# Optimization experiments

Hardware: AMD Instinct MI355X
Metric: run time of the kernel (lower is better)

## Reference

```python
import jax, jax.numpy as jnp
import numpy as np

N = 50000
E = 800000
IN_DIM = 256
HID = 64
HEADS = 4
OUT = 64
NEG_SLOPE = 0.2


def _gat_layer(x, src, dst, W, a_src, a_dst, b, heads, out_ch, concat):
    n = x.shape[0]
    h = (x @ W).reshape(n, heads, out_ch)                      # [N,H,C]
    al_src = jnp.sum(h * a_src, axis=-1)                       # [N,H]
    al_dst = jnp.sum(h * a_dst, axis=-1)                       # [N,H]
    e = jax.nn.leaky_relu(al_src[src] + al_dst[dst], NEG_SLOPE)  # [E,H]
    # segment softmax over destination nodes
    m = jax.ops.segment_max(e, dst, num_segments=n)
    m = jnp.where(jnp.isfinite(m), m, 0.0)
    ex = jnp.exp(e - m[dst])
    denom = jax.ops.segment_sum(ex, dst, num_segments=n)
    alpha = ex / (denom[dst] + 1e-16)                          # [E,H]
    msg = h[src] * alpha[:, :, None]                           # [E,H,C]
    out = jax.ops.segment_sum(msg, dst, num_segments=n)        # [N,H,C]
    out = out.reshape(n, heads * out_ch) if concat else out.mean(axis=1)
    return out + b


def setup_inputs() -> dict:
    key = jax.random.key(0)
    ks = jax.random.split(key, 16)
    x = jax.random.normal(ks[0], (N, IN_DIM), dtype=jnp.float32)
    edge_index = jax.random.randint(ks[1], (2, E), 0, N, dtype=jnp.int64)

    def glorot(k, shape):
        fan = shape[0] + shape[-1]
        s = jnp.sqrt(6.0 / fan).astype(jnp.float32)
        return jax.random.uniform(k, shape, jnp.float32, -s, s)

    # layer 1: IN_DIM -> HID x HEADS (concat)
    W1 = glorot(ks[2], (IN_DIM, HEADS * HID))
    a_src1 = glorot(ks[3], (HEADS, HID))
    a_dst1 = glorot(ks[4], (HEADS, HID))
    b1 = jnp.zeros((HEADS * HID,), jnp.float32)
    # layer 2: HID*HEADS -> HID x HEADS (concat)
    W2 = glorot(ks[5], (HEADS * HID, HEADS * HID))
    a_src2 = glorot(ks[6], (HEADS, HID))
    a_dst2 = glorot(ks[7], (HEADS, HID))
    b2 = jnp.zeros((HEADS * HID,), jnp.float32)
    # layer 3: HID*HEADS -> OUT, 1 head, concat=False
    W3 = glorot(ks[8], (HEADS * HID, OUT))
    a_src3 = glorot(ks[9], (1, OUT))
    a_dst3 = glorot(ks[10], (1, OUT))
    b3 = jnp.zeros((OUT,), jnp.float32)

    return {"x": x, "edge_index": edge_index,
            "W1": W1, "a_src1": a_src1, "a_dst1": a_dst1, "b1": b1,
            "W2": W2, "a_src2": a_src2, "a_dst2": a_dst2, "b2": b2,
            "W3": W3, "a_src3": a_src3, "a_dst3": a_dst3, "b3": b3}


def reference(x, edge_index, W1, a_src1, a_dst1, b1, W2, a_src2, a_dst2, b2, W3, a_src3, a_dst3, b3):
    src, dst = edge_index[0], edge_index[1]
    h = _gat_layer(x, src, dst, W1, a_src1, a_dst1, b1, HEADS, HID, True)
    h = jax.nn.elu(h)
    h = _gat_layer(h, src, dst, W2, a_src2, a_dst2, b2, HEADS, HID, True)
    h = jax.nn.elu(h)
    h = _gat_layer(h, src, dst, W3, a_src3, a_dst3, b3, 1, OUT, False)
    h = jax.nn.elu(h)
    return h
```

## Files before the change

kernel.cpp:

```cpp
#include <hip/hip_runtime.h>
#include <hip/hip_bf16.h>
#include <math.h>

#define IN_DIM 256
#define HID 64
#define HEADS 4
#define HC (HEADS * HID)
#define OUTC 64
#define NEG_SLOPE 0.2f

typedef unsigned int uint;
typedef unsigned short ushortt;
typedef __attribute__((ext_vector_type(8))) short short8v;
typedef __attribute__((ext_vector_type(4))) float floatx4;

union U8 { uint u[4]; short8v v; };

__device__ __forceinline__ float lrelu(float x) {
    return x >= 0.f ? x : NEG_SLOPE * x;
}
__device__ __forceinline__ float elu1(float x) {
    return x > 0.f ? x : expm1f(x);
}
__device__ __forceinline__ ushortt f2bf(float f) {
    uint x = __float_as_uint(f);
    uint r = (x + 0x7fffu + ((x >> 16) & 1u)) >> 16;
    return (ushortt)r;
}
__device__ __forceinline__ float bf2f(ushortt u) {
    return __uint_as_float(((uint)u) << 16);
}

#define CVTPAIR(fx, fy, ho, qo)                                                 \
    asm("v_cvt_pk_bf16_f32 %0, %1, %2" : "=v"(ho) : "v"(fx), "v"(fy));          \
    {                                                                           \
        float _r0 = (fx) - __uint_as_float((ho) << 16);                         \
        float _r1 = (fy) - __uint_as_float((ho) & 0xffff0000u);                 \
        asm("v_cvt_pk_bf16_f32 %0, %1, %2" : "=v"(qo) : "v"(_r0), "v"(_r1));    \
    }

__global__ void count_edges(const int* __restrict__ dst, int* __restrict__ counts, int E) {
    int e = blockIdx.x * blockDim.x + threadIdx.x;
    if (e < E) atomicAdd(&counts[dst[e]], 1);
}

#define SCAN_B 1024
__global__ void scan_block(const int* __restrict__ counts, int* __restrict__ ptr,
                           int* __restrict__ bsums, int n) {
    __shared__ int sm[SCAN_B];
    int b = blockIdx.x, t = threadIdx.x;
    int i = b * SCAN_B + t;
    int v = (i < n) ? counts[i] : 0;
    sm[t] = v;
    __syncthreads();
    for (int off = 1; off < SCAN_B; off <<= 1) {
        int add = (t >= off) ? sm[t - off] : 0;
        __syncthreads();
        sm[t] += add;
        __syncthreads();
    }
    if (i < n) ptr[i + 1] = sm[t];
    if (t == SCAN_B - 1) bsums[b] = sm[t];
}

__global__ void scan_add(int* __restrict__ ptr, const int* __restrict__ bsums,
                         int* __restrict__ work, int n) {
    __shared__ int pre;
    int seg = blockIdx.x >> 2;
    if (threadIdx.x == 0) {
        int s = 0;
        for (int b = 0; b < seg; b++) s += bsums[b];
        pre = s;
    }
    __syncthreads();
    int i = blockIdx.x * 256 + threadIdx.x;
    if (i == 0) { ptr[0] = 0; work[0] = 0; }
    if (i < n) {
        int v = ptr[i + 1] + pre;
        ptr[i + 1] = v;
        if (i + 1 < n) work[i + 1] = v;
    }
}

__global__ void scatter_edges(const int* __restrict__ src, const int* __restrict__ dst,
                              int* __restrict__ work, int* __restrict__ ssrc, int E) {
    int e = blockIdx.x * blockDim.x + threadIdx.x;
    if (e < E) {
        int p = atomicAdd(&work[dst[e]], 1);
        ssrc[p] = src[e] * 64;
    }
}

__device__ __forceinline__ void wsplit_body(const float* __restrict__ W,
                                            ushortt* __restrict__ Wt, int N,
                                            int b, int tid) {
    int idx = b * 256 + tid;
    int j = idx & 7;
    int col = (idx >> 3) % N;
    int kb = (idx >> 3) / N;
    float wv = W[(size_t)(kb * 8 + j) * N + col];
    ushortt hi = f2bf(wv);
    ushortt lo = f2bf(wv - bf2f(hi));
    size_t o = ((size_t)kb * N + col) * 16 + j;
    Wt[o] = hi;
    Wt[o + 8] = lo;
}

__global__ __launch_bounds__(256) void prep(
        const float* __restrict__ W1, const float* __restrict__ W2,
        const float* __restrict__ W3,
        ushortt* __restrict__ Wt1, ushortt* __restrict__ Wt2,
        ushortt* __restrict__ Wt3) {
    int b = blockIdx.x, tid = threadIdx.x;
    if (b < 256) { wsplit_body(W1, Wt1, 256, b, tid); return; }
    if (b < 512) { wsplit_body(W2, Wt2, 256, b - 256, tid); return; }
    wsplit_body(W3, Wt3, 64, b - 512, tid);
}

template<bool F32A>
__global__ __launch_bounds__(256) void gemm_mfma(
        const ushortt* __restrict__ Ai, const float* __restrict__ Af,
        const ushortt* __restrict__ Wt,
        ushortt* __restrict__ Chi, int M,
        const float* __restrict__ a_src, const float* __restrict__ a_dst,
        float* __restrict__ alS, float* __restrict__ alD) {
    constexpr int N = 256;
    int t = threadIdx.x;
    int wid = t >> 6, l = t & 63, l15 = l & 15, chunk = l >> 4;
    int wr = wid >> 1, wc = wid & 1;
    int row0 = blockIdx.x * 64;
    int colw = wc * 128;

    floatx4 acc[2][8];
    floatx4 zero = {0.f, 0.f, 0.f, 0.f};
#pragma unroll
    for (int mt = 0; mt < 2; mt++)
#pragma unroll
        for (int nt = 0; nt < 8; nt++) acc[mt][nt] = zero;

    size_t arow[2];
#pragma unroll
    for (int mt = 0; mt < 2; mt++) {
        int r = row0 + wr * 32 + mt * 16 + l15;
        int rc = r < M ? r : M - 1;
        arow[mt] = F32A ? (size_t)rc * 256 : (size_t)rc * 512;
    }

    for (int ks = 0; ks < 8; ks++) {
        int kb = ks * 4 + chunk;
        short8v ah[2], aq[2];
        if constexpr (F32A) {
#pragma unroll
            for (int mt = 0; mt < 2; mt++) {
                const float* ap = Af + arow[mt] + kb * 8;
                float4 a0 = ((const float4*)ap)[0];
                float4 a1 = ((const float4*)ap)[1];
                U8 h, q;
                CVTPAIR(a0.x, a0.y, h.u[0], q.u[0]);
                CVTPAIR(a0.z, a0.w, h.u[1], q.u[1]);
                CVTPAIR(a1.x, a1.y, h.u[2], q.u[2]);
                CVTPAIR(a1.z, a1.w, h.u[3], q.u[3]);
                ah[mt] = h.v; aq[mt] = q.v;
            }
        } else {
#pragma unroll
            for (int mt = 0; mt < 2; mt++) {
                const ushortt* ap = Ai + arow[mt] + kb * 16;
                ah[mt] = *(const short8v*)ap;
                aq[mt] = *(const short8v*)(ap + 8);
            }
        }
        const ushortt* bbase = Wt + ((size_t)kb * N + colw + l15) * 16;
        short8v bh[8], bq[8];
#pragma unroll
        for (int nt = 0; nt < 8; nt++) {
            const ushortt* bp = bbase + (size_t)nt * 16 * 16;
            bh[nt] = *(const short8v*)bp;
            bq[nt] = *(const short8v*)(bp + 8);
        }
#pragma unroll
        for (int mt = 0; mt < 2; mt++)
#pragma unroll
            for (int nt = 0; nt < 8; nt++) {
                acc[mt][nt] = __builtin_amdgcn_mfma_f32_16x16x32_bf16(aq[mt], bh[nt], acc[mt][nt], 0, 0, 0);
                acc[mt][nt] = __builtin_amdgcn_mfma_f32_16x16x32_bf16(ah[mt], bq[nt], acc[mt][nt], 0, 0, 0);
                acc[mt][nt] = __builtin_amdgcn_mfma_f32_16x16x32_bf16(ah[mt], bh[nt], acc[mt][nt], 0, 0, 0);
            }
    }

#pragma unroll
    for (int mt = 0; mt < 2; mt++)
#pragma unroll
        for (int j = 0; j < 4; j++) {
            int r = row0 + wr * 32 + mt * 16 + chunk * 4 + j;
            if (r < M) {
#pragma unroll
                for (int nt = 0; nt < 8; nt++)
                    Chi[(size_t)r * N + colw + nt * 16 + l15] = f2bf(acc[mt][nt][j]);
            }
        }

    {
        float aSv[8], aDv[8];
#pragma unroll
        for (int nt = 0; nt < 8; nt++) {
            aSv[nt] = a_src[colw + nt * 16 + l15];
            aDv[nt] = a_dst[colw + nt * 16 + l15];
        }
#pragma unroll
        for (int mt = 0; mt < 2; mt++)
#pragma unroll
            for (int j = 0; j < 4; j++) {
                float s0 = 0.f, d0 = 0.f, s1 = 0.f, d1 = 0.f;
#pragma unroll
                for (int nt = 0; nt < 4; nt++) {
                    s0 += acc[mt][nt][j] * aSv[nt];
                    d0 += acc[mt][nt][j] * aDv[nt];
                    s1 += acc[mt][nt + 4][j] * aSv[nt + 4];
                    d1 += acc[mt][nt + 4][j] * aDv[nt + 4];
                }
#pragma unroll
                for (int off = 1; off < 16; off <<= 1) {
                    s0 += __shfl_xor(s0, off);
                    d0 += __shfl_xor(d0, off);
                    s1 += __shfl_xor(s1, off);
                    d1 += __shfl_xor(d1, off);
                }
                int r = row0 + wr * 32 + mt * 16 + chunk * 4 + j;
                if (l15 == 0 && r < M) {
                    alS[(size_t)r * 4 + wc * 2 + 0] = s0;
                    alS[(size_t)r * 4 + wc * 2 + 1] = s1;
                    alD[(size_t)r * 4 + wc * 2 + 0] = d0;
                    alD[(size_t)r * 4 + wc * 2 + 1] = d1;
                }
            }
    }
}

__global__ __launch_bounds__(256) void gemm_n64(
        const ushortt* __restrict__ Ai, const ushortt* __restrict__ Wt,
        ushortt* __restrict__ Chi, int M,
        const float* __restrict__ a_src, const float* __restrict__ a_dst,
        float* __restrict__ alS, float* __restrict__ alD) {
    constexpr int N = 64;
    int t = threadIdx.x;
    int wid = t >> 6, l = t & 63, l15 = l & 15, chunk = l >> 4;
    int row0 = blockIdx.x * 64;
    int rw = row0 + wid * 16 + l15;
    size_t arow = (size_t)(rw < M ? rw : M - 1) * 512;

    floatx4 acc[4];
    floatx4 zero = {0.f, 0.f, 0.f, 0.f};
#pragma unroll
    for (int nt = 0; nt < 4; nt++) acc[nt] = zero;

    for (int ks = 0; ks < 8; ks++) {
        int kb = ks * 4 + chunk;
        short8v bh[4], bq[4];
#pragma unroll
        for (int nt = 0; nt < 4; nt++) {
            const ushortt* bp = Wt + ((size_t)kb * N + nt * 16 + l15) * 16;
            bh[nt] = *(const short8v*)bp;
            bq[nt] = *(const short8v*)(bp + 8);
        }
        const ushortt* ap = Ai + arow + kb * 16;
        short8v ah = *(const short8v*)ap;
        short8v aq = *(const short8v*)(ap + 8);
#pragma unroll
        for (int nt = 0; nt < 4; nt++) {
            acc[nt] = __builtin_amdgcn_mfma_f32_16x16x32_bf16(aq, bh[nt], acc[nt], 0, 0, 0);
            acc[nt] = __builtin_amdgcn_mfma_f32_16x16x32_bf16(ah, bq[nt], acc[nt], 0, 0, 0);
            acc[nt] = __builtin_amdgcn_mfma_f32_16x16x32_bf16(ah, bh[nt], acc[nt], 0, 0, 0);
        }
    }

    float aSv[4], aDv[4];
#pragma unroll
    for (int nt = 0; nt < 4; nt++) {
        aSv[nt] = a_src[nt * 16 + l15];
        aDv[nt] = a_dst[nt * 16 + l15];
    }
#pragma unroll
    for (int j = 0; j < 4; j++) {
        int r = row0 + wid * 16 + chunk * 4 + j;
        if (r < M) {
#pragma unroll
            for (int nt = 0; nt < 4; nt++)
                Chi[(size_t)r * N + nt * 16 + l15] = f2bf(acc[nt][j]);
        }
        float s = 0.f, d = 0.f;
#pragma unroll
        for (int nt = 0; nt < 4; nt++) {
            s += acc[nt][j] * aSv[nt];
            d += acc[nt][j] * aDv[nt];
        }
#pragma unroll
        for (int off = 1; off < 16; off <<= 1) {
            s += __shfl_xor(s, off);
            d += __shfl_xor(d, off);
        }
        if (l15 == 0 && r < M) {
            alS[r] = s;
            alD[r] = d;
        }
    }
}

__global__ __launch_bounds__(256) void gather4f(
        const float* __restrict__ alS, const float* __restrict__ alD,
        const ushortt* __restrict__ h, float* ealpha,
        const int* __restrict__ ptr, const int* __restrict__ ssrc,
        const float* __restrict__ bias, ushortt* __restrict__ outAi, int n) {
    int w = threadIdx.x >> 6, lane = threadIdx.x & 63;
    int node = blockIdx.x * 4 + w;
    if (node >= n) return;
    int p0 = ptr[node], p1 = ptr[node + 1];
    int head = lane >> 4;

    float4 ad = ((const float4*)alD)[node];
    const float4* alS4 = (const float4*)alS;
    float4* e4 = (float4*)ealpha;
    float4 sum = make_float4(0.f, 0.f, 0.f, 0.f);
    for (int i = p0 + lane; i < p1; i += 64) {
        float4 as = alS4[ssrc[i] >> 6];
        float4 e;
        e.x = __expf(lrelu(as.x + ad.x));
        e.y = __expf(lrelu(as.y + ad.y));
        e.z = __expf(lrelu(as.z + ad.z));
        e.w = __expf(lrelu(as.w + ad.w));
        e4[i] = e;
        sum.x += e.x; sum.y += e.y; sum.z += e.z; sum.w += e.w;
    }
#pragma unroll
    for (int off = 1; off < 64; off <<= 1) {
        sum.x += __shfl_xor(sum.x, off);
        sum.y += __shfl_xor(sum.y, off);
        sum.z += __shfl_xor(sum.z, off);
        sum.w += __shfl_xor(sum.w, off);
    }
    float sv = sum.x;
    if (head == 1) sv = sum.y;
    else if (head == 2) sv = sum.z;
    else if (head == 3) sv = sum.w;
    float invh = 1.f / (sv + 1e-16f);

    const float* alpha = ealpha;
    const ushort4* h4 = (const ushort4*)h;
    float4 acc0 = make_float4(0.f, 0.f, 0.f, 0.f);
    float4 acc1 = make_float4(0.f, 0.f, 0.f, 0.f);

    int i = p0;
#pragma unroll 1
    for (; i + 8 <= p1; i += 8) {
        int o0 = ssrc[i+0], o1 = ssrc[i+1], o2 = ssrc[i+2], o3 = ssrc[i+3];
        int o4 = ssrc[i+4], o5 = ssrc[i+5], o6 = ssrc[i+6], o7 = ssrc[i+7];
        float w0 = alpha[(i+0)*4 + head];
        float w1 = alpha[(i+1)*4 + head];
        float w2 = alpha[(i+2)*4 + head];
        float w3 = alpha[(i+3)*4 + head];
        float w4 = alpha[(i+4)*4 + head];
        float w5 = alpha[(i+5)*4 + head];
        float w6 = alpha[(i+6)*4 + head];
        float w7 = alpha[(i+7)*4 + head];
        ushort4 u0 = h4[o0 + lane];
        ushort4 u1 = h4[o1 + lane];
        ushort4 u2 = h4[o2 + lane];
        ushort4 u3 = h4[o3 + lane];
        ushort4 u4 = h4[o4 + lane];
        ushort4 u5 = h4[o5 + lane];
        ushort4 u6 = h4[o6 + lane];
        ushort4 u7 = h4[o7 + lane];
        acc0.x += bf2f(u0.x)*w0; acc0.y += bf2f(u0.y)*w0; acc0.z += bf2f(u0.z)*w0; acc0.w += bf2f(u0.w)*w0;
        acc1.x += bf2f(u1.x)*w1; acc1.y += bf2f(u1.y)*w1; acc1.z += bf2f(u1.z)*w1; acc1.w += bf2f(u1.w)*w1;
        acc0.x += bf2f(u2.x)*w2; acc0.y += bf2f(u2.y)*w2; acc0.z += bf2f(u2.z)*w2; acc0.w += bf2f(u2.w)*w2;
        acc1.x += bf2f(u3.x)*w3; acc1.y += bf2f(u3.y)*w3; acc1.z += bf2f(u3.z)*w3; acc1.w += bf2f(u3.w)*w3;
        acc0.x += bf2f(u4.x)*w4; acc0.y += bf2f(u4.y)*w4; acc0.z += bf2f(u4.z)*w4; acc0.w += bf2f(u4.w)*w4;
        acc1.x += bf2f(u5.x)*w5; acc1.y += bf2f(u5.y)*w5; acc1.z += bf2f(u5.z)*w5; acc1.w += bf2f(u5.w)*w5;
        acc0.x += bf2f(u6.x)*w6; acc0.y += bf2f(u6.y)*w6; acc0.z += bf2f(u6.z)*w6; acc0.w += bf2f(u6.w)*w6;
        acc1.x += bf2f(u7.x)*w7; acc1.y += bf2f(u7.y)*w7; acc1.z += bf2f(u7.z)*w7; acc1.w += bf2f(u7.w)*w7;
    }
#pragma unroll 1
    for (; i < p1; ++i) {
        int o0 = ssrc[i];
        float w0 = alpha[i*4 + head];
        ushort4 u0 = h4[o0 + lane];
        acc0.x += bf2f(u0.x)*w0; acc0.y += bf2f(u0.y)*w0; acc0.z += bf2f(u0.z)*w0; acc0.w += bf2f(u0.w)*w0;
    }
    acc0.x = (acc0.x + acc1.x) * invh;
    acc0.y = (acc0.y + acc1.y) * invh;
    acc0.z = (acc0.z + acc1.z) * invh;
    acc0.w = (acc0.w + acc1.w) * invh;

    float4 b = ((const float4*)bias)[lane];
    float4 o;
    o.x = elu1(acc0.x + b.x);
    o.y = elu1(acc0.y + b.y);
    o.z = elu1(acc0.z + b.z);
    o.w = elu1(acc0.w + b.w);
    ushort4 oh, oq;
    oh.x = f2bf(o.x); oq.x = f2bf(o.x - bf2f(oh.x));
    oh.y = f2bf(o.y); oq.y = f2bf(o.y - bf2f(oh.y));
    oh.z = f2bf(o.z); oq.z = f2bf(o.z - bf2f(oh.z));
    oh.w = f2bf(o.w); oq.w = f2bf(o.w - bf2f(oh.w));
    size_t base = (size_t)node * 512 + (lane >> 1) * 16 + (lane & 1) * 4;
    *(ushort4*)&outAi[base] = oh;
    *(ushort4*)&outAi[base + 8] = oq;
}

__global__ __launch_bounds__(256) void gather1f(
        const float* __restrict__ alS, const float* __restrict__ alD,
        const ushortt* __restrict__ h, float* ealpha,
        const int* __restrict__ ptr, const int* __restrict__ ssrc,
        const float* __restrict__ bias, float* __restrict__ out, int n) {
    int w = threadIdx.x >> 6, lane = threadIdx.x & 63;
    int node = blockIdx.x * 4 + w;
    if (node >= n) return;
    int p0 = ptr[node], p1 = ptr[node + 1];

    float ad = alD[node];
    float sum = 0.f;
    for (int i = p0 + lane; i < p1; i += 64) {
        float e = __expf(lrelu(alS[ssrc[i] >> 6] + ad));
        ealpha[i] = e;
        sum += e;
    }
#pragma unroll
    for (int off = 1; off < 64; off <<= 1) sum += __shfl_xor(sum, off);
    float inv = 1.f / (sum + 1e-16f);

    int eslot = lane >> 4, cg = lane & 15;
    const float* alpha = ealpha;
    const ushort4* h4 = (const ushort4*)h;
    float4 acc = make_float4(0.f, 0.f, 0.f, 0.f);

#pragma unroll 1
    for (int i = p0 + eslot; i < p1; i += 4) {
        int o = ssrc[i];
        float wv = alpha[i];
        ushort4 u = h4[(o >> 2) + cg];
        acc.x += bf2f(u.x) * wv;
        acc.y += bf2f(u.y) * wv;
        acc.z += bf2f(u.z) * wv;
        acc.w += bf2f(u.w) * wv;
    }
#pragma unroll
    for (int off = 16; off < 64; off <<= 1) {
        acc.x += __shfl_xor(acc.x, off);
        acc.y += __shfl_xor(acc.y, off);
        acc.z += __shfl_xor(acc.z, off);
        acc.w += __shfl_xor(acc.w, off);
    }
    if (eslot == 0) {
        float4 b = ((const float4*)bias)[cg];
        float4 o;
        o.x = elu1(acc.x * inv + b.x);
        o.y = elu1(acc.y * inv + b.y);
        o.z = elu1(acc.z * inv + b.z);
        o.w = elu1(acc.w * inv + b.w);
        ((float4*)out)[node * 16 + cg] = o;
    }
}

extern "C" void kernel_launch(void* const* d_in, const int* in_sizes, int n_in,
                              void* d_out, int out_size, void* d_ws, size_t ws_size,
                              hipStream_t stream) {
    const float* x      = (const float*)d_in[0];
    const int*   eidx   = (const int*)d_in[1];
    const float* W1     = (const float*)d_in[2];
    const float* a_src1 = (const float*)d_in[3];
    const float* a_dst1 = (const float*)d_in[4];
    const float* b1     = (const float*)d_in[5];
    const float* W2     = (const float*)d_in[6];
    const float* a_src2 = (const float*)d_in[7];
    const float* a_dst2 = (const float*)d_in[8];
    const float* b2     = (const float*)d_in[9];
    const float* W3     = (const float*)d_in[10];
    const float* a_src3 = (const float*)d_in[11];
    const float* a_dst3 = (const float*)d_in[12];
    const float* b3     = (const float*)d_in[13];

    const int n = in_sizes[0] / IN_DIM;
    const int E = in_sizes[1] / 2;
    const int* srcp = eidx;
    const int* dstp = eidx + E;

    size_t off = 0;
    auto alloc = [&](size_t bytes) {
        void* p = (char*)d_ws + off;
        off += (bytes + 255) & ~(size_t)255;
        return p;
    };
    int*     ptr    = (int*)alloc((size_t)(n + 1) * 4);
    int*     work   = (int*)alloc((size_t)n * 4);
    int*     bsums  = (int*)alloc(256 * 4);
    int*     ssrc   = (int*)alloc((size_t)E * 4);
    ushortt* Ai0    = (ushortt*)alloc((size_t)n * 512 * 2);
    ushortt* Ai1    = (ushortt*)alloc((size_t)n * 512 * 2);
    ushortt* hbf    = (ushortt*)alloc((size_t)n * HC * 2);
    float*   alS    = (float*)alloc((size_t)n * HEADS * 4);
    float*   alD    = (float*)alloc((size_t)n * HEADS * 4);
    float*   ealpha = (float*)alloc((size_t)E * HEADS * 4);
    ushortt* Wt1    = (ushortt*)alloc((size_t)256 * HC * 2 * 2);
    ushortt* Wt2    = (ushortt*)alloc((size_t)256 * HC * 2 * 2);
    ushortt* Wt3    = (ushortt*)alloc((size_t)256 * OUTC * 2 * 2);
    (void)ws_size;

    hipMemsetAsync(work, 0, (size_t)n * 4, stream);
    count_edges<<<(E + 255) / 256, 256, 0, stream>>>(dstp, work, E);
    int nb = (n + SCAN_B - 1) / SCAN_B;
    scan_block<<<nb, SCAN_B, 0, stream>>>(work, ptr, bsums, n);
    scan_add<<<(n + 255) / 256, 256, 0, stream>>>(ptr, bsums, work, n);
    scatter_edges<<<(E + 255) / 256, 256, 0, stream>>>(srcp, dstp, work, ssrc, E);

    prep<<<576, 256, 0, stream>>>(W1, W2, W3, Wt1, Wt2, Wt3);

    int gblocks = (n + 63) / 64;
    int node4 = (n + 3) / 4;

    gemm_mfma<true><<<gblocks, 256, 0, stream>>>(
        nullptr, x, Wt1, hbf, n, a_src1, a_dst1, alS, alD);
    gather4f<<<node4, 256, 0, stream>>>(alS, alD, hbf, ealpha, ptr, ssrc, b1, Ai1, n);

    gemm_mfma<false><<<gblocks, 256, 0, stream>>>(
        Ai1, nullptr, Wt2, hbf, n, a_src2, a_dst2, alS, alD);
    gather4f<<<node4, 256, 0, stream>>>(alS, alD, hbf, ealpha, ptr, ssrc, b2, Ai0, n);

    gemm_n64<<<gblocks, 256, 0, stream>>>(
        Ai0, Wt3, hbf, n, a_src3, a_dst3, alS, alD);
    gather1f<<<node4, 256, 0, stream>>>(alS, alD, hbf, ealpha, ptr, ssrc, b3,
                                        (float*)d_out, n);
}
```

Measured before the change: 402.1 us.

## Fuse softmax weights into gather loops and merge weight prep with edge counting

```diff
diff --git a/kernel.cpp b/kernel.cpp
--- a/kernel.cpp
+++ b/kernel.cpp
@@ -39,8 +39,32 @@
         asm("v_cvt_pk_bf16_f32 %0, %1, %2" : "=v"(qo) : "v"(_r0), "v"(_r1));    \
     }
 
-__global__ void count_edges(const int* __restrict__ dst, int* __restrict__ counts, int E) {
-    int e = blockIdx.x * blockDim.x + threadIdx.x;
+__device__ __forceinline__ void wsplit_body(const float* __restrict__ W,
+                                            ushortt* __restrict__ Wt, int N,
+                                            int b, int tid) {
+    int idx = b * 256 + tid;
+    int j = idx & 7;
+    int col = (idx >> 3) % N;
+    int kb = (idx >> 3) / N;
+    float wv = W[(size_t)(kb * 8 + j) * N + col];
+    ushortt hi = f2bf(wv);
+    ushortt lo = f2bf(wv - bf2f(hi));
+    size_t o = ((size_t)kb * N + col) * 16 + j;
+    Wt[o] = hi;
+    Wt[o + 8] = lo;
+}
+
+__global__ __launch_bounds__(256) void count_prep(
+        const float* __restrict__ W1, const float* __restrict__ W2,
+        const float* __restrict__ W3,
+        ushortt* __restrict__ Wt1, ushortt* __restrict__ Wt2,
+        ushortt* __restrict__ Wt3,
+        const int* __restrict__ dst, int* __restrict__ counts, int E) {
+    int b = blockIdx.x, tid = threadIdx.x;
+    if (b < 256) { wsplit_body(W1, Wt1, 256, b, tid); return; }
+    if (b < 512) { wsplit_body(W2, Wt2, 256, b - 256, tid); return; }
+    if (b < 576) { wsplit_body(W3, Wt3, 64, b - 512, tid); return; }
+    int e = (b - 576) * 256 + tid;
     if (e < E) atomicAdd(&counts[dst[e]], 1);
 }
 
@@ -91,32 +115,6 @@
     }
 }
 
-__device__ __forceinline__ void wsplit_body(const float* __restrict__ W,
-                                            ushortt* __restrict__ Wt, int N,
-                                            int b, int tid) {
-    int idx = b * 256 + tid;
-    int j = idx & 7;
-    int col = (idx >> 3) % N;
-    int kb = (idx >> 3) / N;
-    float wv = W[(size_t)(kb * 8 + j) * N + col];
-    ushortt hi = f2bf(wv);
-    ushortt lo = f2bf(wv - bf2f(hi));
-    size_t o = ((size_t)kb * N + col) * 16 + j;
-    Wt[o] = hi;
-    Wt[o + 8] = lo;
-}
-
-__global__ __launch_bounds__(256) void prep(
-        const float* __restrict__ W1, const float* __restrict__ W2,
-        const float* __restrict__ W3,
-        ushortt* __restrict__ Wt1, ushortt* __restrict__ Wt2,
-        ushortt* __restrict__ Wt3) {
-    int b = blockIdx.x, tid = threadIdx.x;
-    if (b < 256) { wsplit_body(W1, Wt1, 256, b, tid); return; }
-    if (b < 512) { wsplit_body(W2, Wt2, 256, b - 256, tid); return; }
-    wsplit_body(W3, Wt3, 64, b - 512, tid);
-}
-
 template<bool F32A>
 __global__ __launch_bounds__(256) void gemm_mfma(
         const ushortt* __restrict__ Ai, const float* __restrict__ Af,
@@ -308,7 +306,7 @@
 
 __global__ __launch_bounds__(256) void gather4f(
         const float* __restrict__ alS, const float* __restrict__ alD,
-        const ushortt* __restrict__ h, float* ealpha,
+        const ushortt* __restrict__ h,
         const int* __restrict__ ptr, const int* __restrict__ ssrc,
         const float* __restrict__ bias, ushortt* __restrict__ outAi, int n) {
     int w = threadIdx.x >> 6, lane = threadIdx.x & 63;
@@ -316,52 +314,25 @@
     if (node >= n) return;
     int p0 = ptr[node], p1 = ptr[node + 1];
     int head = lane >> 4;
-
-    float4 ad = ((const float4*)alD)[node];
-    const float4* alS4 = (const float4*)alS;
-    float4* e4 = (float4*)ealpha;
-    float4 sum = make_float4(0.f, 0.f, 0.f, 0.f);
-    for (int i = p0 + lane; i < p1; i += 64) {
-        float4 as = alS4[ssrc[i] >> 6];
-        float4 e;
-        e.x = __expf(lrelu(as.x + ad.x));
-        e.y = __expf(lrelu(as.y + ad.y));
-        e.z = __expf(lrelu(as.z + ad.z));
-        e.w = __expf(lrelu(as.w + ad.w));
-        e4[i] = e;
-        sum.x += e.x; sum.y += e.y; sum.z += e.z; sum.w += e.w;
-    }
-#pragma unroll
-    for (int off = 1; off < 64; off <<= 1) {
-        sum.x += __shfl_xor(sum.x, off);
-        sum.y += __shfl_xor(sum.y, off);
-        sum.z += __shfl_xor(sum.z, off);
-        sum.w += __shfl_xor(sum.w, off);
-    }
-    float sv = sum.x;
-    if (head == 1) sv = sum.y;
-    else if (head == 2) sv = sum.z;
-    else if (head == 3) sv = sum.w;
-    float invh = 1.f / (sv + 1e-16f);
-
-    const float* alpha = ealpha;
+    float adh = alD[node * 4 + head];
     const ushort4* h4 = (const ushort4*)h;
     float4 acc0 = make_float4(0.f, 0.f, 0.f, 0.f);
     float4 acc1 = make_float4(0.f, 0.f, 0.f, 0.f);
+    float sum = 0.f;
 
     int i = p0;
 #pragma unroll 1
     for (; i + 8 <= p1; i += 8) {
         int o0 = ssrc[i+0], o1 = ssrc[i+1], o2 = ssrc[i+2], o3 = ssrc[i+3];
         int o4 = ssrc[i+4], o5 = ssrc[i+5], o6 = ssrc[i+6], o7 = ssrc[i+7];
-        float w0 = alpha[(i+0)*4 + head];
-        float w1 = alpha[(i+1)*4 + head];
-        float w2 = alpha[(i+2)*4 + head];
-        float w3 = alpha[(i+3)*4 + head];
-        float w4 = alpha[(i+4)*4 + head];
-        float w5 = alpha[(i+5)*4 + head];
-        float w6 = alpha[(i+6)*4 + head];
-        float w7 = alpha[(i+7)*4 + head];
+        float w0 = __expf(lrelu(alS[(o0 >> 4) + head] + adh));
+        float w1 = __expf(lrelu(alS[(o1 >> 4) + head] + adh));
+        float w2 = __expf(lrelu(alS[(o2 >> 4) + head] + adh));
+        float w3 = __expf(lrelu(alS[(o3 >> 4) + head] + adh));
+        float w4 = __expf(lrelu(alS[(o4 >> 4) + head] + adh));
+        float w5 = __expf(lrelu(alS[(o5 >> 4) + head] + adh));
+        float w6 = __expf(lrelu(alS[(o6 >> 4) + head] + adh));
+        float w7 = __expf(lrelu(alS[(o7 >> 4) + head] + adh));
         ushort4 u0 = h4[o0 + lane];
         ushort4 u1 = h4[o1 + lane];
         ushort4 u2 = h4[o2 + lane];
@@ -370,6 +341,7 @@
         ushort4 u5 = h4[o5 + lane];
         ushort4 u6 = h4[o6 + lane];
         ushort4 u7 = h4[o7 + lane];
+        sum += w0 + w1 + w2 + w3 + w4 + w5 + w6 + w7;
         acc0.x += bf2f(u0.x)*w0; acc0.y += bf2f(u0.y)*w0; acc0.z += bf2f(u0.z)*w0; acc0.w += bf2f(u0.w)*w0;
         acc1.x += bf2f(u1.x)*w1; acc1.y += bf2f(u1.y)*w1; acc1.z += bf2f(u1.z)*w1; acc1.w += bf2f(u1.w)*w1;
         acc0.x += bf2f(u2.x)*w2; acc0.y += bf2f(u2.y)*w2; acc0.z += bf2f(u2.z)*w2; acc0.w += bf2f(u2.w)*w2;
@@ -382,10 +354,12 @@
 #pragma unroll 1
     for (; i < p1; ++i) {
         int o0 = ssrc[i];
-        float w0 = alpha[i*4 + head];
+        float w0 = __expf(lrelu(alS[(o0 >> 4) + head] + adh));
         ushort4 u0 = h4[o0 + lane];
+        sum += w0;
         acc0.x += bf2f(u0.x)*w0; acc0.y += bf2f(u0.y)*w0; acc0.z += bf2f(u0.z)*w0; acc0.w += bf2f(u0.w)*w0;
     }
+    float invh = 1.f / (sum + 1e-16f);
     acc0.x = (acc0.x + acc1.x) * invh;
     acc0.y = (acc0.y + acc1.y) * invh;
     acc0.z = (acc0.z + acc1.z) * invh;
@@ -409,35 +383,25 @@
 
 __global__ __launch_bounds__(256) void gather1f(
         const float* __restrict__ alS, const float* __restrict__ alD,
-        const ushortt* __restrict__ h, float* ealpha,
+        const ushortt* __restrict__ h,
         const int* __restrict__ ptr, const int* __restrict__ ssrc,
         const float* __restrict__ bias, float* __restrict__ out, int n) {
     int w = threadIdx.x >> 6, lane = threadIdx.x & 63;
     int node = blockIdx.x * 4 + w;
     if (node >= n) return;
     int p0 = ptr[node], p1 = ptr[node + 1];
-
     float ad = alD[node];
-    float sum = 0.f;
-    for (int i = p0 + lane; i < p1; i += 64) {
-        float e = __expf(lrelu(alS[ssrc[i] >> 6] + ad));
-        ealpha[i] = e;
-        sum += e;
-    }
-#pragma unroll
-    for (int off = 1; off < 64; off <<= 1) sum += __shfl_xor(sum, off);
-    float inv = 1.f / (sum + 1e-16f);
-
     int eslot = lane >> 4, cg = lane & 15;
-    const float* alpha = ealpha;
     const ushort4* h4 = (const ushort4*)h;
     float4 acc = make_float4(0.f, 0.f, 0.f, 0.f);
+    float sum = 0.f;
 
 #pragma unroll 1
     for (int i = p0 + eslot; i < p1; i += 4) {
         int o = ssrc[i];
-        float wv = alpha[i];
+        float wv = __expf(lrelu(alS[o >> 6] + ad));
         ushort4 u = h4[(o >> 2) + cg];
+        sum += wv;
         acc.x += bf2f(u.x) * wv;
         acc.y += bf2f(u.y) * wv;
         acc.z += bf2f(u.z) * wv;
@@ -449,8 +413,10 @@
         acc.y += __shfl_xor(acc.y, off);
         acc.z += __shfl_xor(acc.z, off);
         acc.w += __shfl_xor(acc.w, off);
+        sum   += __shfl_xor(sum, off);
     }
     if (eslot == 0) {
+        float inv = 1.f / (sum + 1e-16f);
         float4 b = ((const float4*)bias)[cg];
         float4 o;
         o.x = elu1(acc.x * inv + b.x);
@@ -499,34 +465,33 @@
     ushortt* hbf    = (ushortt*)alloc((size_t)n * HC * 2);
     float*   alS    = (float*)alloc((size_t)n * HEADS * 4);
     float*   alD    = (float*)alloc((size_t)n * HEADS * 4);
-    float*   ealpha = (float*)alloc((size_t)E * HEADS * 4);
     ushortt* Wt1    = (ushortt*)alloc((size_t)256 * HC * 2 * 2);
     ushortt* Wt2    = (ushortt*)alloc((size_t)256 * HC * 2 * 2);
     ushortt* Wt3    = (ushortt*)alloc((size_t)256 * OUTC * 2 * 2);
     (void)ws_size;
 
     hipMemsetAsync(work, 0, (size_t)n * 4, stream);
-    count_edges<<<(E + 255) / 256, 256, 0, stream>>>(dstp, work, E);
+    int cblocks = 576 + (E + 255) / 256;
+    count_prep<<<cblocks, 256, 0, stream>>>(W1, W2, W3, Wt1, Wt2, Wt3,
+                                            dstp, work, E);
     int nb = (n + SCAN_B - 1) / SCAN_B;
     scan_block<<<nb, SCAN_B, 0, stream>>>(work, ptr, bsums, n);
     scan_add<<<(n + 255) / 256, 256, 0, stream>>>(ptr, bsums, work, n);
     scatter_edges<<<(E + 255) / 256, 256, 0, stream>>>(srcp, dstp, work, ssrc, E);
 
-    prep<<<576, 256, 0, stream>>>(W1, W2, W3, Wt1, Wt2, Wt3);
-
     int gblocks = (n + 63) / 64;
     int node4 = (n + 3) / 4;
 
     gemm_mfma<true><<<gblocks, 256, 0, stream>>>(
         nullptr, x, Wt1, hbf, n, a_src1, a_dst1, alS, alD);
-    gather4f<<<node4, 256, 0, stream>>>(alS, alD, hbf, ealpha, ptr, ssrc, b1, Ai1, n);
+    gather4f<<<node4, 256, 0, stream>>>(alS, alD, hbf, ptr, ssrc, b1, Ai1, n);
 
     gemm_mfma<false><<<gblocks, 256, 0, stream>>>(
         Ai1, nullptr, Wt2, hbf, n, a_src2, a_dst2, alS, alD);
-    gather4f<<<node4, 256, 0, stream>>>(alS, alD, hbf, ealpha, ptr, ssrc, b2, Ai0, n);
+    gather4f<<<node4, 256, 0, stream>>>(alS, alD, hbf, ptr, ssrc, b2, Ai0, n);
 
     gemm_n64<<<gblocks, 256, 0, stream>>>(
         Ai0, Wt3, hbf, n, a_src3, a_dst3, alS, alD);
-    gather1f<<<node4, 256, 0, stream>>>(alS, alD, hbf, ealpha, ptr, ssrc, b3,
+    gather1f<<<node4, 256, 0, stream>>>(alS, alD, hbf, ptr, ssrc, b3,
                                         (float*)d_out, n);
 }
```

After: 387.3 us. 3.7% less time.
